# Kernel optimization log

Measured on AMD Instinct MI355X. Metric: run time of the kernel, lower is better.

## Reference

```python
import jax, jax.numpy as jnp
import numpy as np

E, H, I, K, T = 8, 1024, 2816, 2, 2048


def setup_inputs() -> dict:
    key = jax.random.key(0)
    k1, k2, k3, k4, k5, k6 = jax.random.split(key, 6)
    hidden_states = jax.random.normal(k1, (T, H), dtype=jnp.float32)
    top_k_indices = jax.random.randint(k2, (T, K), 0, E, dtype=jnp.int32)
    raw = jax.random.uniform(k3, (T, K), dtype=jnp.float32) + 0.1
    top_k_values = raw / jnp.sum(raw, axis=-1, keepdims=True)  # router softmax-like weights
    scale = 1.0 / np.sqrt(H)
    w_gate = jax.random.normal(k4, (E, H, I), dtype=jnp.float32) * scale
    w_up = jax.random.normal(k5, (E, H, I), dtype=jnp.float32) * scale
    w_down = jax.random.normal(k6, (E, I, H), dtype=jnp.float32) * (1.0 / np.sqrt(I))
    return {
        "hidden_states": hidden_states,
        "top_k_indices": top_k_indices,
        "top_k_values": top_k_values,
        "w_gate": w_gate,
        "w_up": w_up,
        "w_down": w_down,
    }


def reference(hidden_states, top_k_indices, top_k_values, w_gate, w_up, w_down):
    # Each expert: SwiGLU FFN  down( silu(x @ gate) * (x @ up) )
    # Run every expert on every token (dense reference for grouped-GEMM dispatch),
    # then combine with the per-token top-k routing weights.
    def expert(wg, wu, wd):
        g = jnp.matmul(hidden_states, wg)          # [T, I]
        u = jnp.matmul(hidden_states, wu)          # [T, I]
        return jnp.matmul(jax.nn.silu(g) * u, wd)  # [T, H]

    y = jax.vmap(expert)(w_gate, w_up, w_down)     # [E, T, H]

    t = hidden_states.shape[0]
    # comb[t, e] = sum over k of top_k_values[t, k] where top_k_indices[t, k] == e
    comb = jnp.zeros((t, w_gate.shape[0]), dtype=hidden_states.dtype)
    comb = comb.at[jnp.arange(t)[:, None], top_k_indices].add(top_k_values)
    out = jnp.einsum('te,eth->th', comb, y)        # weighted combine -> [T, H]
    return out
```

## Files before the change

### kernel.cpp

```cpp
#include <hip/hip_runtime.h>
#include <stdint.h>

#define T_TOK 2048
#define KTOP  2
#define NEXP  8
#define HDIM  1024
#define IDIM  2816

#define NPAIR 4096

#define BM        128
#define MAX_TILES 40
#define NPP       (NPAIR + BM)
#define BN2       128
#define BK2       32
#define BN3       64
#define BK3       64

#define R1BM   256
#define R1T    24
#define R1NPP  (NPAIR + R1BM)
#define R1BN2  128
#define R1BK2  32
#define R1BKp2 40
#define R1BN3  64
#define R1BK3  64
#define R1BKp3 72

typedef __attribute__((ext_vector_type(8))) short short8;
typedef __attribute__((ext_vector_type(4))) float floatx4;

__device__ __forceinline__ unsigned short f2bf(float f) {
  unsigned int u = __float_as_uint(f);
  u += 0x7fffu + ((u >> 16) & 1u);
  return (unsigned short)(u >> 16);
}

__device__ __forceinline__ void glds16(const unsigned short* g, unsigned short* l) {
  __builtin_amdgcn_global_load_lds(
      (const __attribute__((address_space(1))) unsigned int*)g,
      (__attribute__((address_space(3))) unsigned int*)l, 16, 0, 0);
}

__global__ void setup_kernel(const int* __restrict__ idx,
                             const float* __restrict__ vals,
                             int* __restrict__ hdr,
                             int* __restrict__ stok,
                             float* __restrict__ sw, int bm) {
  __shared__ int cnt[NEXP];
  __shared__ int off[NEXP];
  int tid = threadIdx.x;
  if (tid < NEXP) cnt[tid] = 0;
  __syncthreads();
  for (int p = tid; p < NPAIR; p += blockDim.x) atomicAdd(&cnt[idx[p]], 1);
  __syncthreads();
  if (tid == 0) {
    int s = 0, nt = 0;
    for (int e = 0; e < NEXP; ++e) {
      off[e] = s;
      int n = cnt[e];
      for (int t0 = 0; t0 < n; t0 += bm) {
        hdr[nt] = e;
        hdr[64 + nt] = s + t0;
        hdr[128 + nt] = s + n;
        nt++;
      }
      s += n;
    }
    for (; nt < 64; ++nt) hdr[nt] = -1;
  }
  __syncthreads();
  for (int p = tid; p < NPAIR; p += blockDim.x) {
    int e = idx[p];
    int pos = atomicAdd(&off[e], 1);
    stok[pos] = p / KTOP;
    sw[pos] = vals[p];
  }
}

__global__ void gather_kernel(const float* __restrict__ hidden,
                              const int* __restrict__ stok,
                              unsigned short* __restrict__ Xs) {
  int p = blockIdx.x;
  int t = stok[p];
  const float4* src = reinterpret_cast<const float4*>(hidden + (size_t)t * HDIM);
  float4 v = src[threadIdx.x];
  uint2 q;
  q.x = f2bf(v.x) | ((unsigned)f2bf(v.y) << 16);
  q.y = f2bf(v.z) | ((unsigned)f2bf(v.w) << 16);
  *reinterpret_cast<uint2*>(Xs + (size_t)p * HDIM + threadIdx.x * 4) = q;
}

__global__ __launch_bounds__(256) void convert_kernel(
    const float* __restrict__ wg, const float* __restrict__ wu,
    const float* __restrict__ wd, unsigned short* __restrict__ wgT,
    unsigned short* __restrict__ wuT, unsigned short* __restrict__ wdT,
    int zoff) {
  __shared__ float ls[64][65];
  int z = blockIdx.z + zoff;
  int e = blockIdx.y;
  int M = (z == 2) ? IDIM : HDIM;
  int N = (z == 2) ? HDIM : IDIM;
  const float* src = (z == 0 ? wg : z == 1 ? wu : wd) + (size_t)e * M * N;
  unsigned short* dst = (z == 0 ? wgT : z == 1 ? wuT : wdT) + (size_t)e * M * N;
  int ntx = N >> 6;
  int n0 = (blockIdx.x % ntx) << 6;
  int m0 = (blockIdx.x / ntx) << 6;
  int t = threadIdx.x;
  int rr = t >> 4, cc = (t & 15) * 4;
#pragma unroll
  for (int i = 0; i < 4; ++i) {
    int r = rr + i * 16;
    float4 v = *reinterpret_cast<const float4*>(src + (size_t)(m0 + r) * N + n0 + cc);
    ls[r][cc] = v.x; ls[r][cc + 1] = v.y; ls[r][cc + 2] = v.z; ls[r][cc + 3] = v.w;
  }
  __syncthreads();
  int mc = (t & 7) * 8, nn = t >> 3;
#pragma unroll
  for (int i = 0; i < 2; ++i) {
    int n = nn + i * 32;
    uint4 q;
    q.x = f2bf(ls[mc][n])     | ((unsigned)f2bf(ls[mc + 1][n]) << 16);
    q.y = f2bf(ls[mc + 2][n]) | ((unsigned)f2bf(ls[mc + 3][n]) << 16);
    q.z = f2bf(ls[mc + 4][n]) | ((unsigned)f2bf(ls[mc + 5][n]) << 16);
    q.w = f2bf(ls[mc + 6][n]) | ((unsigned)f2bf(ls[mc + 7][n]) << 16);
    *reinterpret_cast<uint4*>(dst + (size_t)(n0 + n) * M + m0 + mc) = q;
  }
}

__global__ __launch_bounds__(256, 2) void gateup_kernel(
    const unsigned short* __restrict__ Xs, const unsigned short* __restrict__ wgT,
    const unsigned short* __restrict__ wuT, const int* __restrict__ hdr,
    const float* __restrict__ sw_g, unsigned short* __restrict__ Act) {
  int bx = blockIdx.x;
  int e = hdr[bx];
  if (e < 0) return;
  int row0 = hdr[64 + bx];
  int rowlim = hdr[128 + bx] - row0;
  int n0 = blockIdx.y * BN2;

  __shared__ __align__(16) unsigned short As[BM * BK2];
  __shared__ __align__(16) unsigned short Bg[BN2 * BK2];
  __shared__ __align__(16) unsigned short Bu[BN2 * BK2];
  __shared__ float sw[BM];

  int tid = threadIdx.x, lane = tid & 63, wave = tid >> 6;
  if (tid < BM) sw[tid] = sw_g[row0 + tid];

  const unsigned short* wgb = wgT + (size_t)e * IDIM * HDIM;
  const unsigned short* wub = wuT + (size_t)e * IDIM * HDIM;

  floatx4 accg[4][4], accu[4][4];
  floatx4 zz = {0.f, 0.f, 0.f, 0.f};
#pragma unroll
  for (int a = 0; a < 4; ++a)
#pragma unroll
    for (int b = 0; b < 4; ++b) { accg[a][b] = zz; accu[a][b] = zz; }

  int wm = (wave >> 1) * 64, wn = (wave & 1) * 64;
  int lr = lane >> 2;
  int lk = (((lane & 3) ^ ((lr >> 1) & 3)) * 8);
  int fr = lane & 15;
  int fq = (((lane >> 4) ^ ((fr >> 1) & 3)) * 8);

  for (int kb = 0; kb < HDIM; kb += BK2) {
#pragma unroll
    for (int it = 0; it < 2; ++it) {
      int c = wave * 2 + it;
      glds16(Xs  + (size_t)(row0 + c * 16 + lr) * HDIM + kb + lk, &As[c * 512]);
      glds16(wgb + (size_t)(n0  + c * 16 + lr) * HDIM + kb + lk, &Bg[c * 512]);
      glds16(wub + (size_t)(n0  + c * 16 + lr) * HDIM + kb + lk, &Bu[c * 512]);
    }
    __syncthreads();

    short8 af[4], bg8[4], bu8[4];
#pragma unroll
    for (int x = 0; x < 4; ++x) {
      af[x]  = *reinterpret_cast<const short8*>(&As[(wm + x * 16 + fr) * BK2 + fq]);
      bg8[x] = *reinterpret_cast<const short8*>(&Bg[(wn + x * 16 + fr) * BK2 + fq]);
      bu8[x] = *reinterpret_cast<const short8*>(&Bu[(wn + x * 16 + fr) * BK2 + fq]);
    }
#pragma unroll
    for (int tm = 0; tm < 4; ++tm)
#pragma unroll
      for (int tn = 0; tn < 4; ++tn) {
        accg[tm][tn] = __builtin_amdgcn_mfma_f32_16x16x32_bf16(af[tm], bg8[tn], accg[tm][tn], 0, 0, 0);
        accu[tm][tn] = __builtin_amdgcn_mfma_f32_16x16x32_bf16(af[tm], bu8[tn], accu[tm][tn], 0, 0, 0);
      }
    __syncthreads();
  }

#pragma unroll
  for (int tm = 0; tm < 4; ++tm)
#pragma unroll
    for (int tn = 0; tn < 4; ++tn)
#pragma unroll
      for (int r = 0; r < 4; ++r) {
        int rl = wm + tm * 16 + (lane >> 4) * 4 + r;
        if (rl < rowlim) {
          int col = n0 + wn + tn * 16 + fr;
          float g = accg[tm][tn][r];
          float u = accu[tm][tn][r];
          float s = g / (1.f + __expf(-g));
          Act[(size_t)(row0 + rl) * IDIM + col] = f2bf(s * u * sw[rl]);
        }
      }
}

__global__ __launch_bounds__(256, 3) void down_kernel(
    const unsigned short* __restrict__ Act, const unsigned short* __restrict__ wdT,
    const int* __restrict__ hdr, const int* __restrict__ stok,
    float* __restrict__ out) {
  int bx = blockIdx.x;
  int e = hdr[bx];
  if (e < 0) return;
  int row0 = hdr[64 + bx];
  int rowlim = hdr[128 + bx] - row0;
  int n0 = blockIdx.y * BN3;

  __shared__ __align__(16) unsigned short As[BM * BK3];
  __shared__ __align__(16) unsigned short Bd[BN3 * BK3];
  __shared__ int stk[BM];

  int tid = threadIdx.x, lane = tid & 63, wave = tid >> 6;
  if (tid < BM) stk[tid] = stok[row0 + tid];

  const unsigned short* wdb = wdT + (size_t)e * HDIM * IDIM;

  floatx4 acc[4][2];
  floatx4 zz = {0.f, 0.f, 0.f, 0.f};
#pragma unroll
  for (int a = 0; a < 4; ++a) { acc[a][0] = zz; acc[a][1] = zz; }

  int wm = (wave >> 1) * 64, wn = (wave & 1) * 32;
  int lr8 = lane >> 3;
  int lk8 = (((lane & 7) ^ lr8) * 8);
  int fr = lane & 15;
  int fk = fr & 7;

  for (int kb = 0; kb < IDIM; kb += BK3) {
#pragma unroll
    for (int it = 0; it < 4; ++it) {
      int c = wave * 4 + it;
      glds16(Act + (size_t)(row0 + c * 8 + lr8) * IDIM + kb + lk8, &As[c * 512]);
    }
#pragma unroll
    for (int it = 0; it < 2; ++it) {
      int c = wave * 2 + it;
      glds16(wdb + (size_t)(n0 + c * 8 + lr8) * IDIM + kb + lk8, &Bd[c * 512]);
    }
    __syncthreads();

#pragma unroll
    for (int ks = 0; ks < BK3; ks += 32) {
      int q8 = (ks >> 3) + (lane >> 4);
      int fo = ((q8 ^ fk) * 8);
      short8 af[4], bd8[2];
#pragma unroll
      for (int x = 0; x < 4; ++x)
        af[x] = *reinterpret_cast<const short8*>(&As[(wm + x * 16 + fr) * BK3 + fo]);
#pragma unroll
      for (int x = 0; x < 2; ++x)
        bd8[x] = *reinterpret_cast<const short8*>(&Bd[(wn + x * 16 + fr) * BK3 + fo]);
#pragma unroll
      for (int tm = 0; tm < 4; ++tm)
#pragma unroll
        for (int tn = 0; tn < 2; ++tn)
          acc[tm][tn] = __builtin_amdgcn_mfma_f32_16x16x32_bf16(af[tm], bd8[tn], acc[tm][tn], 0, 0, 0);
    }
    __syncthreads();
  }

#pragma unroll
  for (int tm = 0; tm < 4; ++tm)
#pragma unroll
    for (int tn = 0; tn < 2; ++tn)
#pragma unroll
      for (int r = 0; r < 4; ++r) {
        int rl = wm + tm * 16 + (lane >> 4) * 4 + r;
        if (rl < rowlim) {
          int col = n0 + wn + tn * 16 + fr;
          unsafeAtomicAdd(&out[(size_t)stk[rl] * HDIM + col], acc[tm][tn][r]);
        }
      }
}

__global__ __launch_bounds__(512, 2) void gateup_fb(
    const unsigned short* __restrict__ Xs, const float* __restrict__ wg,
    const float* __restrict__ wu, const int* __restrict__ hdr,
    const float* __restrict__ sw_g, unsigned short* __restrict__ Act) {
  int by = blockIdx.y;
  int e = hdr[by];
  if (e < 0) return;
  int row0 = hdr[64 + by];
  int row_end = hdr[128 + by];
  int n0 = blockIdx.x * R1BN2;

  __shared__ __align__(16) unsigned short As[R1BM * R1BKp2];
  __shared__ __align__(16) unsigned short Bg[R1BN2 * R1BKp2];
  __shared__ __align__(16) unsigned short Bu[R1BN2 * R1BKp2];
  __shared__ float sw[R1BM];

  int tid = threadIdx.x, lane = tid & 63, wave = tid >> 6;
  if (tid < R1BM) sw[tid] = sw_g[row0 + tid];

  const float* wgb = wg + (size_t)e * HDIM * IDIM;
  const float* wub = wu + (size_t)e * HDIM * IDIM;

  floatx4 accg[4][4], accu[4][4];
  floatx4 zz = {0.f, 0.f, 0.f, 0.f};
#pragma unroll
  for (int a = 0; a < 4; ++a)
#pragma unroll
    for (int b = 0; b < 4; ++b) { accg[a][b] = zz; accu[a][b] = zz; }

  int wm = (wave >> 1) * 64, wn = (wave & 1) * 64;

  for (int kb = 0; kb < HDIM; kb += R1BK2) {
    __syncthreads();
#pragma unroll
    for (int it = 0; it < 2; ++it) {
      int cc = wave * 2 + it;
      int m = cc * 16 + (lane >> 2);
      int k = (lane & 3) * 8;
      uint4 v = *reinterpret_cast<const uint4*>(Xs + (size_t)(row0 + m) * HDIM + kb + k);
      *reinterpret_cast<uint4*>(&As[m * R1BKp2 + k]) = v;
    }
#pragma unroll
    for (int it = 0; it < 2; ++it) {
      int cc = wave * 2 + it;
      const float* wb = (cc & 8) ? wub : wgb;
      unsigned short* Bs = (cc & 8) ? Bu : Bg;
      int r = cc & 7;
      int kblk = r >> 1, nh = r & 1;
      int n = nh * 64 + lane;
      int k = kblk * 8;
      const float* src = wb + (size_t)(kb + k) * IDIM + n0 + n;
      uint4 q;
      q.x = f2bf(src[0])                | ((unsigned)f2bf(src[(size_t)IDIM])     << 16);
      q.y = f2bf(src[2 * (size_t)IDIM]) | ((unsigned)f2bf(src[3 * (size_t)IDIM]) << 16);
      q.z = f2bf(src[4 * (size_t)IDIM]) | ((unsigned)f2bf(src[5 * (size_t)IDIM]) << 16);
      q.w = f2bf(src[6 * (size_t)IDIM]) | ((unsigned)f2bf(src[7 * (size_t)IDIM]) << 16);
      *reinterpret_cast<uint4*>(&Bs[n * R1BKp2 + k]) = q;
    }
    __syncthreads();

    int krd = (lane >> 4) * 8;
    short8 af[4], bgf[4], buf_[4];
#pragma unroll
    for (int tm = 0; tm < 4; ++tm)
      af[tm] = *reinterpret_cast<const short8*>(&As[(wm + tm * 16 + (lane & 15)) * R1BKp2 + krd]);
#pragma unroll
    for (int tn = 0; tn < 4; ++tn) {
      bgf[tn]  = *reinterpret_cast<const short8*>(&Bg[(wn + tn * 16 + (lane & 15)) * R1BKp2 + krd]);
      buf_[tn] = *reinterpret_cast<const short8*>(&Bu[(wn + tn * 16 + (lane & 15)) * R1BKp2 + krd]);
    }
#pragma unroll
    for (int tm = 0; tm < 4; ++tm)
#pragma unroll
      for (int tn = 0; tn < 4; ++tn) {
        accg[tm][tn] = __builtin_amdgcn_mfma_f32_16x16x32_bf16(af[tm], bgf[tn], accg[tm][tn], 0, 0, 0);
        accu[tm][tn] = __builtin_amdgcn_mfma_f32_16x16x32_bf16(af[tm], buf_[tn], accu[tm][tn], 0, 0, 0);
      }
  }

  int rowlim = row_end - row0;
#pragma unroll
  for (int tm = 0; tm < 4; ++tm)
#pragma unroll
    for (int tn = 0; tn < 4; ++tn)
#pragma unroll
      for (int r = 0; r < 4; ++r) {
        int rl = wm + tm * 16 + (lane >> 4) * 4 + r;
        if (rl < rowlim) {
          int col = n0 + wn + tn * 16 + (lane & 15);
          float g = accg[tm][tn][r];
          float u = accu[tm][tn][r];
          float s = g / (1.f + __expf(-g));
          Act[(size_t)(row0 + rl) * IDIM + col] = f2bf(s * u * sw[rl]);
        }
      }
}

__global__ __launch_bounds__(512, 2) void down_fb(
    const unsigned short* __restrict__ Act, const float* __restrict__ wd,
    const int* __restrict__ hdr, const int* __restrict__ stok,
    float* __restrict__ out) {
  int by = blockIdx.y;
  int e = hdr[by];
  if (e < 0) return;
  int row0 = hdr[64 + by];
  int row_end = hdr[128 + by];
  int n0 = blockIdx.x * R1BN3;

  __shared__ __align__(16) unsigned short As[R1BM * R1BKp3];
  __shared__ __align__(16) unsigned short Bd[R1BN3 * R1BKp3];
  __shared__ int stk[R1BM];

  int tid = threadIdx.x, lane = tid & 63, wave = tid >> 6;
  if (tid < R1BM) stk[tid] = stok[row0 + tid];

  const float* wdb = wd + (size_t)e * IDIM * HDIM;

  floatx4 acc[4][2];
  floatx4 zz = {0.f, 0.f, 0.f, 0.f};
#pragma unroll
  for (int a = 0; a < 4; ++a) { acc[a][0] = zz; acc[a][1] = zz; }

  int wm = (wave >> 1) * 64, wn = (wave & 1) * 32;

  for (int kb = 0; kb < IDIM; kb += R1BK3) {
    __syncthreads();
#pragma unroll
    for (int it = 0; it < 4; ++it) {
      int cc = wave * 4 + it;
      int m = cc * 8 + (lane >> 3);
      int k = (lane & 7) * 8;
      uint4 v = *reinterpret_cast<const uint4*>(Act + (size_t)(row0 + m) * IDIM + kb + k);
      *reinterpret_cast<uint4*>(&As[m * R1BKp3 + k]) = v;
    }
    {
      int n = lane;
      int k = wave * 8;
      const float* src = wdb + (size_t)(kb + k) * HDIM + n0 + n;
      uint4 q;
      q.x = f2bf(src[0])        | ((unsigned)f2bf(src[HDIM])     << 16);
      q.y = f2bf(src[2 * HDIM]) | ((unsigned)f2bf(src[3 * HDIM]) << 16);
      q.z = f2bf(src[4 * HDIM]) | ((unsigned)f2bf(src[5 * HDIM]) << 16);
      q.w = f2bf(src[6 * HDIM]) | ((unsigned)f2bf(src[7 * HDIM]) << 16);
      *reinterpret_cast<uint4*>(&Bd[n * R1BKp3 + k]) = q;
    }
    __syncthreads();

#pragma unroll
    for (int ks = 0; ks < R1BK3; ks += 32) {
      int krd = ks + (lane >> 4) * 8;
      short8 af[4], bdf[2];
#pragma unroll
      for (int tm = 0; tm < 4; ++tm)
        af[tm] = *reinterpret_cast<const short8*>(&As[(wm + tm * 16 + (lane & 15)) * R1BKp3 + krd]);
#pragma unroll
      for (int tn = 0; tn < 2; ++tn)
        bdf[tn] = *reinterpret_cast<const short8*>(&Bd[(wn + tn * 16 + (lane & 15)) * R1BKp3 + krd]);
#pragma unroll
      for (int tm = 0; tm < 4; ++tm)
#pragma unroll
        for (int tn = 0; tn < 2; ++tn)
          acc[tm][tn] = __builtin_amdgcn_mfma_f32_16x16x32_bf16(af[tm], bdf[tn], acc[tm][tn], 0, 0, 0);
    }
  }

  int rowlim = row_end - row0;
#pragma unroll
  for (int tm = 0; tm < 4; ++tm)
#pragma unroll
    for (int tn = 0; tn < 2; ++tn)
#pragma unroll
      for (int r = 0; r < 4; ++r) {
        int rl = wm + tm * 16 + (lane >> 4) * 4 + r;
        if (rl < rowlim) {
          int col = n0 + wn + tn * 16 + (lane & 15);
          unsafeAtomicAdd(&out[(size_t)stk[rl] * HDIM + col], acc[tm][tn][r]);
        }
      }
}

extern "C" void kernel_launch(void* const* d_in, const int* in_sizes, int n_in,
                              void* d_out, int out_size, void* d_ws, size_t ws_size,
                              hipStream_t stream) {
  const float* hidden = (const float*)d_in[0];
  const int* idx = (const int*)d_in[1];
  const float* vals = (const float*)d_in[2];
  const float* wg = (const float*)d_in[3];
  const float* wu = (const float*)d_in[4];
  const float* wd = (const float*)d_in[5];
  float* out = (float*)d_out;
  char* ws = (char*)d_ws;

  hipMemsetAsync(d_out, 0, (size_t)out_size * sizeof(float), stream);

  const size_t OFF_STOK = 4096;
  const size_t OFF_SW   = OFF_STOK + (size_t)NPP * 4;
  const size_t OFF_XS   = 65536;
  const size_t OFF_ACT  = OFF_XS + (size_t)NPP * HDIM * 2;
  const size_t OFF_WG   = OFF_ACT + (size_t)NPP * IDIM * 2;
  const size_t WSZ      = (size_t)NEXP * HDIM * IDIM * 2;
  const size_t OFF_WU   = OFF_WG + WSZ;
  const size_t NEED     = OFF_WU + WSZ;

  if (ws_size >= NEED) {
    int* hdr = (int*)ws;
    int* stok = (int*)(ws + OFF_STOK);
    float* sw = (float*)(ws + OFF_SW);
    unsigned short* Xs  = (unsigned short*)(ws + OFF_XS);
    unsigned short* Act = (unsigned short*)(ws + OFF_ACT);
    unsigned short* wgT = (unsigned short*)(ws + OFF_WG);
    unsigned short* wuT = (unsigned short*)(ws + OFF_WU);
    unsigned short* wdT = wgT;

    setup_kernel<<<1, 256, 0, stream>>>(idx, vals, hdr, stok, sw, BM);
    convert_kernel<<<dim3(704, NEXP, 2), 256, 0, stream>>>(wg, wu, wd, wgT, wuT, wdT, 0);
    gather_kernel<<<NPAIR, 256, 0, stream>>>(hidden, stok, Xs);
    gateup_kernel<<<dim3(MAX_TILES, IDIM / BN2), 256, 0, stream>>>(Xs, wgT, wuT, hdr, sw, Act);
    convert_kernel<<<dim3(704, NEXP, 1), 256, 0, stream>>>(wg, wu, wd, wgT, wuT, wdT, 2);
    down_kernel<<<dim3(MAX_TILES, HDIM / BN3), 256, 0, stream>>>(Act, wdT, hdr, stok, out);
  } else {
    int* hdr = (int*)ws;
    int* stok = (int*)(ws + 4096);
    float* sw = (float*)(ws + 4096 + (size_t)R1NPP * 4);
    unsigned short* Xs  = (unsigned short*)(ws + 65536);
    unsigned short* Act = (unsigned short*)(ws + 65536 + (size_t)R1NPP * HDIM * 2);

    setup_kernel<<<1, 256, 0, stream>>>(idx, vals, hdr, stok, sw, R1BM);
    gather_kernel<<<NPAIR, 256, 0, stream>>>(hidden, stok, Xs);
    gateup_fb<<<dim3(IDIM / R1BN2, R1T), 512, 0, stream>>>(Xs, wg, wu, hdr, sw, Act);
    down_fb<<<dim3(HDIM / R1BN3, R1T), 512, 0, stream>>>(Act, wd, hdr, stok, out);
  }
}
```

Baseline: 451.8 us.

## Fuse down-weight conversion into gate/up launch, remap tiles per XCD, packed bf16

When the workspace is large enough, the down-projection weights are converted into a separate buffer by extra blocks appended to the gate/up GEMM grid. This lets the conversion overlap with the GEMM instead of running as its own serialized launch. The change also remaps tile indices so neighbouring tiles land on the same XCD, uses the hardware packed bf16 convert instruction, and widens the setup kernel to 1024 threads. The costs are more workspace, a 1D grid whose tiles are decoded by hand, and a dependence on inline asm.

```diff
diff --git a/kernel.cpp b/kernel.cpp
--- a/kernel.cpp
+++ b/kernel.cpp
@@ -16,6 +16,8 @@
 #define BK2       32
 #define BN3       64
 #define BK3       64
+#define GUB       (MAX_TILES * (IDIM / BN2))
+#define CVB       ((IDIM / 64) * (HDIM / 64) * NEXP)
 
 #define R1BM   256
 #define R1T    24
@@ -36,10 +38,20 @@
   return (unsigned short)(u >> 16);
 }
 
+__device__ __forceinline__ unsigned int pkbf(float a, float b) {
+  unsigned int r;
+  asm volatile("v_cvt_pk_bf16_f32 %0, %1, %2" : "=v"(r) : "v"(a), "v"(b));
+  return r;
+}
+
 __device__ __forceinline__ void glds16(const unsigned short* g, unsigned short* l) {
   __builtin_amdgcn_global_load_lds(
       (const __attribute__((address_space(1))) unsigned int*)g,
       (__attribute__((address_space(3))) unsigned int*)l, 16, 0, 0);
+}
+
+__device__ __forceinline__ int xcd_tile(int bx0) {
+  return (bx0 & 7) * (MAX_TILES / 8) + (bx0 >> 3);
 }
 
 __global__ void setup_kernel(const int* __restrict__ idx,
@@ -86,8 +98,8 @@
   const float4* src = reinterpret_cast<const float4*>(hidden + (size_t)t * HDIM);
   float4 v = src[threadIdx.x];
   uint2 q;
-  q.x = f2bf(v.x) | ((unsigned)f2bf(v.y) << 16);
-  q.y = f2bf(v.z) | ((unsigned)f2bf(v.w) << 16);
+  q.x = pkbf(v.x, v.y);
+  q.y = pkbf(v.z, v.w);
   *reinterpret_cast<uint2*>(Xs + (size_t)p * HDIM + threadIdx.x * 4) = q;
 }
 
@@ -120,10 +132,10 @@
   for (int i = 0; i < 2; ++i) {
     int n = nn + i * 32;
     uint4 q;
-    q.x = f2bf(ls[mc][n])     | ((unsigned)f2bf(ls[mc + 1][n]) << 16);
-    q.y = f2bf(ls[mc + 2][n]) | ((unsigned)f2bf(ls[mc + 3][n]) << 16);
-    q.z = f2bf(ls[mc + 4][n]) | ((unsigned)f2bf(ls[mc + 5][n]) << 16);
-    q.w = f2bf(ls[mc + 6][n]) | ((unsigned)f2bf(ls[mc + 7][n]) << 16);
+    q.x = pkbf(ls[mc][n],     ls[mc + 1][n]);
+    q.y = pkbf(ls[mc + 2][n], ls[mc + 3][n]);
+    q.z = pkbf(ls[mc + 4][n], ls[mc + 5][n]);
+    q.w = pkbf(ls[mc + 6][n], ls[mc + 7][n]);
     *reinterpret_cast<uint4*>(dst + (size_t)(n0 + n) * M + m0 + mc) = q;
   }
 }
@@ -131,18 +143,56 @@
 __global__ __launch_bounds__(256, 2) void gateup_kernel(
     const unsigned short* __restrict__ Xs, const unsigned short* __restrict__ wgT,
     const unsigned short* __restrict__ wuT, const int* __restrict__ hdr,
-    const float* __restrict__ sw_g, unsigned short* __restrict__ Act) {
-  int bx = blockIdx.x;
+    const float* __restrict__ sw_g, unsigned short* __restrict__ Act,
+    const float* __restrict__ wd, unsigned short* __restrict__ wdT) {
+  __shared__ __align__(16) char smem[25088];
+
+  if (blockIdx.x >= GUB) {
+    int cb = blockIdx.x - GUB;
+    int e = cb / ((IDIM / 64) * (HDIM / 64));
+    int bq = cb % ((IDIM / 64) * (HDIM / 64));
+    const int ntx = HDIM >> 6;
+    int n0 = (bq % ntx) << 6;
+    int m0 = (bq / ntx) << 6;
+    const float* src = wd + (size_t)e * IDIM * HDIM;
+    unsigned short* dst = wdT + (size_t)e * IDIM * HDIM;
+    float (*ls)[65] = reinterpret_cast<float(*)[65]>(smem);
+    int t = threadIdx.x;
+    int rr = t >> 4, cc = (t & 15) * 4;
+#pragma unroll
+    for (int i = 0; i < 4; ++i) {
+      int r = rr + i * 16;
+      float4 v = *reinterpret_cast<const float4*>(src + (size_t)(m0 + r) * HDIM + n0 + cc);
+      ls[r][cc] = v.x; ls[r][cc + 1] = v.y; ls[r][cc + 2] = v.z; ls[r][cc + 3] = v.w;
+    }
+    __syncthreads();
+    int mc = (t & 7) * 8, nn = t >> 3;
+#pragma unroll
+    for (int i = 0; i < 2; ++i) {
+      int n = nn + i * 32;
+      uint4 q;
+      q.x = pkbf(ls[mc][n],     ls[mc + 1][n]);
+      q.y = pkbf(ls[mc + 2][n], ls[mc + 3][n]);
+      q.z = pkbf(ls[mc + 4][n], ls[mc + 5][n]);
+      q.w = pkbf(ls[mc + 6][n], ls[mc + 7][n]);
+      *reinterpret_cast<uint4*>(dst + (size_t)(n0 + n) * IDIM + m0 + mc) = q;
+    }
+    return;
+  }
+
+  int mx = blockIdx.x % MAX_TILES;
+  int ny = blockIdx.x / MAX_TILES;
+  int bx = xcd_tile(mx);
   int e = hdr[bx];
   if (e < 0) return;
   int row0 = hdr[64 + bx];
   int rowlim = hdr[128 + bx] - row0;
-  int n0 = blockIdx.y * BN2;
-
-  __shared__ __align__(16) unsigned short As[BM * BK2];
-  __shared__ __align__(16) unsigned short Bg[BN2 * BK2];
-  __shared__ __align__(16) unsigned short Bu[BN2 * BK2];
-  __shared__ float sw[BM];
+  int n0 = ny * BN2;
+
+  unsigned short* As = reinterpret_cast<unsigned short*>(smem);
+  unsigned short* Bg = reinterpret_cast<unsigned short*>(smem + 8192);
+  unsigned short* Bu = reinterpret_cast<unsigned short*>(smem + 16384);
+  float* sw = reinterpret_cast<float*>(smem + 24576);
 
   int tid = threadIdx.x, lane = tid & 63, wave = tid >> 6;
   if (tid < BM) sw[tid] = sw_g[row0 + tid];
@@ -211,7 +261,7 @@
     const unsigned short* __restrict__ Act, const unsigned short* __restrict__ wdT,
     const int* __restrict__ hdr, const int* __restrict__ stok,
     float* __restrict__ out) {
-  int bx = blockIdx.x;
+  int bx = xcd_tile(blockIdx.x);
   int e = hdr[bx];
   if (e < 0) return;
   int row0 = hdr[64 + bx];
@@ -486,7 +536,9 @@
   const size_t OFF_WG   = OFF_ACT + (size_t)NPP * IDIM * 2;
   const size_t WSZ      = (size_t)NEXP * HDIM * IDIM * 2;
   const size_t OFF_WU   = OFF_WG + WSZ;
-  const size_t NEED     = OFF_WU + WSZ;
+  const size_t OFF_WD   = OFF_WU + WSZ;
+  const size_t NEED     = OFF_WD;
+  const size_t NEED2    = OFF_WD + WSZ;
 
   if (ws_size >= NEED) {
     int* hdr = (int*)ws;
@@ -496,13 +548,18 @@
     unsigned short* Act = (unsigned short*)(ws + OFF_ACT);
     unsigned short* wgT = (unsigned short*)(ws + OFF_WG);
     unsigned short* wuT = (unsigned short*)(ws + OFF_WU);
-    unsigned short* wdT = wgT;
-
-    setup_kernel<<<1, 256, 0, stream>>>(idx, vals, hdr, stok, sw, BM);
+    bool sep = (ws_size >= NEED2);
+    unsigned short* wdT = sep ? (unsigned short*)(ws + OFF_WD) : wgT;
+
+    setup_kernel<<<1, 1024, 0, stream>>>(idx, vals, hdr, stok, sw, BM);
     convert_kernel<<<dim3(704, NEXP, 2), 256, 0, stream>>>(wg, wu, wd, wgT, wuT, wdT, 0);
     gather_kernel<<<NPAIR, 256, 0, stream>>>(hidden, stok, Xs);
-    gateup_kernel<<<dim3(MAX_TILES, IDIM / BN2), 256, 0, stream>>>(Xs, wgT, wuT, hdr, sw, Act);
-    convert_kernel<<<dim3(704, NEXP, 1), 256, 0, stream>>>(wg, wu, wd, wgT, wuT, wdT, 2);
+    if (sep) {
+      gateup_kernel<<<GUB + CVB, 256, 0, stream>>>(Xs, wgT, wuT, hdr, sw, Act, wd, wdT);
+    } else {
+      gateup_kernel<<<GUB, 256, 0, stream>>>(Xs, wgT, wuT, hdr, sw, Act, wd, wdT);
+      convert_kernel<<<dim3(704, NEXP, 1), 256, 0, stream>>>(wg, wu, wd, wgT, wuT, wdT, 2);
+    }
     down_kernel<<<dim3(MAX_TILES, HDIM / BN3), 256, 0, stream>>>(Act, wdT, hdr, stok, out);
   } else {
     int* hdr = (int*)ws;
@@ -511,7 +568,7 @@
     unsigned short* Xs  = (unsigned short*)(ws + 65536);
     unsigned short* Act = (unsigned short*)(ws + 65536 + (size_t)R1NPP * HDIM * 2);
 
-    setup_kernel<<<1, 256, 0, stream>>>(idx, vals, hdr, stok, sw, R1BM);
+    setup_kernel<<<1, 1024, 0, stream>>>(idx, vals, hdr, stok, sw, R1BM);
     gather_kernel<<<NPAIR, 256, 0, stream>>>(hidden, stok, Xs);
     gateup_fb<<<dim3(IDIM / R1BN2, R1T), 512, 0, stream>>>(Xs, wg, wu, hdr, sw, Act);
     down_fb<<<dim3(HDIM / R1BN3, R1T), 512, 0, stream>>>(Act, wd, hdr, stok, out);
```

Measured after the change: 420.3 us. 7.0% less time.
